# Kernel tuning notes

Hardware: AMD Instinct MI355X
Metric: run time of the kernel (lower is better)

## Reference

```python
import jax, jax.numpy as jnp
import numpy as np

D_MODEL = 1024
N_HEADS = 16
D_HEAD = D_MODEL // N_HEADS
ROPE_BASE = 10000.0


def _rotate_half(x):
    half = x.shape[-1] // 2
    x1, x2 = x[..., :half], x[..., half:]
    return jnp.concatenate([-x2, x1], axis=-1)


def _rope_cos_sin(seq_len, d_head, dtype):
    inv_freq = 1.0 / (ROPE_BASE ** (jnp.arange(0, d_head, 2, dtype=jnp.float32) / d_head))
    t = jnp.arange(seq_len, dtype=jnp.float32)
    freqs = jnp.outer(t, inv_freq)                       # [S, d_head/2]
    emb = jnp.concatenate([freqs, freqs], axis=-1)       # [S, d_head]
    return jnp.cos(emb).astype(dtype), jnp.sin(emb).astype(dtype)


def setup_inputs() -> dict:
    key = jax.random.key(0)
    k1, k2, k3 = jax.random.split(key, 3)
    B, S = 2, 2048
    x = jax.random.normal(k1, (B, S, D_MODEL), dtype=jnp.float32)
    # torch nn.Linear weight layout: [out_features, in_features], y = x @ W.T
    w_qkv = jax.random.normal(k2, (3 * D_MODEL, D_MODEL), dtype=jnp.float32) * (D_MODEL ** -0.5)
    w_out = jax.random.normal(k3, (D_MODEL, D_MODEL), dtype=jnp.float32) * (D_MODEL ** -0.5)
    return {"x": x, "w_qkv": w_qkv, "w_out": w_out}


def reference(x, w_qkv, w_out):
    B, S, _ = x.shape
    qkv = jnp.einsum('bsd,ed->bse', x, w_qkv)            # [B, S, 3*D]
    qkv = qkv.reshape(B, S, 3, N_HEADS, D_HEAD)
    qkv = jnp.transpose(qkv, (2, 0, 3, 1, 4))            # [3, B, H, S, Dh]
    q, k, v = qkv[0], qkv[1], qkv[2]

    cos, sin = _rope_cos_sin(S, D_HEAD, x.dtype)         # [S, Dh] each
    cos = cos[None, None]                                # [1, 1, S, Dh]
    sin = sin[None, None]
    q = q * cos + _rotate_half(q) * sin
    k = k * cos + _rotate_half(k) * sin

    scale = 1.0 / jnp.sqrt(jnp.array(D_HEAD, dtype=x.dtype))
    attn = jnp.einsum('bhqd,bhkd->bhqk', q, k) * scale   # [B, H, S, S]
    causal = jnp.tril(jnp.ones((S, S), dtype=bool))      # triu(diag=1) masked -> keep lower tri
    attn = jnp.where(causal[None, None], attn, jnp.finfo(x.dtype).min)
    attn = jax.nn.softmax(attn, axis=-1)

    out = jnp.einsum('bhqk,bhkd->bhqd', attn, v)         # [B, H, S, Dh]
    out = jnp.transpose(out, (0, 2, 1, 3)).reshape(B, S, D_MODEL)
    return jnp.einsum('bsd,ed->bse', out, w_out)         # out_proj
```

## Files before the change

### kernel.cpp

```cpp
#include <hip/hip_runtime.h>
#include <hip/hip_bf16.h>
#include <cmath>

#define DMODEL 1024
#define NH 16
#define DH 64
#define SEQ 2048
#define BATCH 2

typedef __attribute__((ext_vector_type(8))) short bf16x8;
typedef __attribute__((ext_vector_type(4))) float f32x4;
typedef __attribute__((ext_vector_type(4))) unsigned int u32x4;
typedef __attribute__((ext_vector_type(8))) unsigned short u16x8;

__device__ __forceinline__ unsigned short f2bf(float f) {
    unsigned int u = __builtin_bit_cast(unsigned int, f);
    u += 0x7fffu + ((u >> 16) & 1u);
    return (unsigned short)(u >> 16);
}
__device__ __forceinline__ float exp2_fast(float x) {
    float r;
    asm("v_exp_f32 %0, %1" : "=v"(r) : "v"(x));
    return r;
}

__global__ __launch_bounds__(256)
void cast_all(const float* __restrict__ x, const float* __restrict__ wq,
              const float* __restrict__ wo, unsigned short* __restrict__ xb,
              unsigned short* __restrict__ wqb, unsigned short* __restrict__ wob)
{
    const int i = blockIdx.x * 256 + threadIdx.x;
    const float* src; unsigned short* dst; int off;
    if (i < 524288)      { src = x;  dst = xb;  off = i; }
    else if (i < 917504) { src = wq; dst = wqb; off = i - 524288; }
    else                 { src = wo; dst = wob; off = i - 917504; }
    const float4 a = *(const float4*)(src + (size_t)off * 8);
    const float4 b = *(const float4*)(src + (size_t)off * 8 + 4);
    u16x8 o;
    o[0] = f2bf(a.x); o[1] = f2bf(a.y); o[2] = f2bf(a.z); o[3] = f2bf(a.w);
    o[4] = f2bf(b.x); o[5] = f2bf(b.y); o[6] = f2bf(b.z); o[7] = f2bf(b.w);
    *(u16x8*)(dst + (size_t)off * 8) = o;
}

template<int BM, int EPI>
__global__ __launch_bounds__(256)
void gemm_bf16(const unsigned short* __restrict__ A,
               const unsigned short* __restrict__ B,
               float* __restrict__ oc, unsigned short* __restrict__ oq,
               unsigned short* __restrict__ ok, unsigned short* __restrict__ ovt,
               int M, int N)
{
    constexpr int K = 1024;
    constexpr int BK = 32;
    constexpr int NT = K / BK;
    constexpr int FM = BM / 32;
    __shared__ unsigned short As[2][BM * BK];
    __shared__ unsigned short Bs[2][128 * BK];

    const int t  = threadIdx.x;
    const int l  = t & 63;
    const int w  = t >> 6;
    const int g  = l >> 4;
    const int ln = l & 15;
    const int wr = w >> 1, wc = w & 1;
    const int m0 = blockIdx.y * BM;
    const int n0 = blockIdx.x * 128;

    auto stage = [&](int kt, int bufi) {
        #pragma unroll
        for (int i = 0; i < BM / 64; ++i) {
            const int n = i * 256 + t;
            const int r = n >> 2, slot = n & 3;
            const int kk = kt * BK + ((slot ^ ((r >> 1) & 3)) * 8);
            const unsigned short* ga = A + (size_t)(m0 + r) * K + kk;
            __builtin_amdgcn_global_load_lds(
                (const __attribute__((address_space(1))) unsigned int*)ga,
                (__attribute__((address_space(3))) unsigned int*)&As[bufi][n * 8], 16, 0, 0);
        }
        #pragma unroll
        for (int i = 0; i < 2; ++i) {
            const int n = i * 256 + t;
            const int r = n >> 2, slot = n & 3;
            const int kk = kt * BK + ((slot ^ ((r >> 1) & 3)) * 8);
            const unsigned short* gb = B + (size_t)(n0 + r) * K + kk;
            __builtin_amdgcn_global_load_lds(
                (const __attribute__((address_space(1))) unsigned int*)gb,
                (__attribute__((address_space(3))) unsigned int*)&Bs[bufi][n * 8], 16, 0, 0);
        }
    };

    f32x4 acc[FM][4];
    #pragma unroll
    for (int i = 0; i < FM; ++i)
        #pragma unroll
        for (int j = 0; j < 4; ++j) acc[i][j] = (f32x4){0.f, 0.f, 0.f, 0.f};

    const int swz = (g ^ ((ln >> 1) & 3)) << 4;

    stage(0, 0);
    for (int kt = 0; kt < NT; ++kt) {
        __syncthreads();
        if (kt + 1 < NT) stage(kt + 1, (kt + 1) & 1);
        const char* as = (const char*)As[kt & 1];
        const char* bs = (const char*)Bs[kt & 1];
        bf16x8 af[FM], bfr[4];
        #pragma unroll
        for (int fm = 0; fm < FM; ++fm)
            af[fm] = *(const bf16x8*)(as + (wr * (BM / 2) + fm * 16 + ln) * 64 + swz);
        #pragma unroll
        for (int fn = 0; fn < 4; ++fn)
            bfr[fn] = *(const bf16x8*)(bs + (wc * 64 + fn * 16 + ln) * 64 + swz);
        #pragma unroll
        for (int fm = 0; fm < FM; ++fm)
            #pragma unroll
            for (int fn = 0; fn < 4; ++fn)
                acc[fm][fn] = __builtin_amdgcn_mfma_f32_16x16x32_bf16(
                    af[fm], bfr[fn], acc[fm][fn], 0, 0, 0);
    }

    const int rowbase = m0 + wr * (BM / 2);
    const int colbase = n0 + wc * 64;
    if (EPI == 1) {
        #pragma unroll
        for (int fm = 0; fm < FM; ++fm)
            #pragma unroll
            for (int fn = 0; fn < 4; ++fn)
                #pragma unroll
                for (int rr = 0; rr < 4; ++rr) {
                    const int row = rowbase + fm * 16 + g * 4 + rr;
                    oc[(size_t)row * N + colbase + fn * 16 + ln] = acc[fm][fn][rr];
                }
    } else {
        const int which = colbase >> 10;
        const int h = (colbase >> 6) & (NH - 1);
        if (which < 2) {
            unsigned short* dst = which == 0 ? oq : ok;
            const float scale = which == 0 ? 0.18033688011112042f : 1.f;
            const float cexp = -13.287712379549449f / 32.f;
            const float if0 = exp2f((float)ln * cexp);
            const float if1 = exp2f((float)(16 + ln) * cexp);
            #pragma unroll
            for (int fm = 0; fm < FM; ++fm)
                #pragma unroll
                for (int rr = 0; rr < 4; ++rr) {
                    const int row = rowbase + fm * 16 + g * 4 + rr;
                    const int b = row >> 11, s = row & (SEQ - 1);
                    float s0, c0, s1, c1;
                    __sincosf((float)s * if0, &s0, &c0);
                    __sincosf((float)s * if1, &s1, &c1);
                    const float x0 = acc[fm][0][rr], x1 = acc[fm][1][rr];
                    const float x2 = acc[fm][2][rr], x3 = acc[fm][3][rr];
                    const size_t base = (((size_t)b * NH + h) * SEQ + s) * DH;
                    dst[base + ln]      = f2bf((x0 * c0 - x2 * s0) * scale);
                    dst[base + 16 + ln] = f2bf((x1 * c1 - x3 * s1) * scale);
                    dst[base + 32 + ln] = f2bf((x2 * c0 + x0 * s0) * scale);
                    dst[base + 48 + ln] = f2bf((x3 * c1 + x1 * s1) * scale);
                }
        } else {
            #pragma unroll
            for (int fm = 0; fm < FM; ++fm)
                #pragma unroll
                for (int fn = 0; fn < 4; ++fn) {
                    const int row = rowbase + fm * 16 + g * 4;
                    const int b = row >> 11, s = row & (SEQ - 1);
                    const int d = fn * 16 + ln;
                    ushort4 pk;
                    pk.x = f2bf(acc[fm][fn][0]); pk.y = f2bf(acc[fm][fn][1]);
                    pk.z = f2bf(acc[fm][fn][2]); pk.w = f2bf(acc[fm][fn][3]);
                    *(ushort4*)&ovt[(((size_t)b * NH + h) * DH + d) * SEQ + s] = pk;
                }
        }
    }
}

__global__ __launch_bounds__(256)
void attn_mfma(const unsigned short* __restrict__ q,
               const unsigned short* __restrict__ k,
               const unsigned short* __restrict__ vt,
               unsigned short* __restrict__ ob)
{
    __shared__ unsigned short Ks[2][64 * 64];
    __shared__ unsigned short Vs[2][64 * 64];

    const int t  = threadIdx.x;
    const int l  = t & 63;
    const int w  = t >> 6;
    const int g  = l >> 4;
    const int ln = l & 15;
    const int bid = blockIdx.x;
    const int xcd = bid & 7, jj = bid >> 3;
    const int bh = xcd * 4 + (jj >> 4);
    const int pi = jj & 15;
    const int qtA = pi, qtB = 31 - pi;
    const size_t bqk = (size_t)bh * SEQ * DH;
    const size_t bv  = (size_t)bh * DH * SEQ;

    bf16x8 qfA0, qfA1, qfB0, qfB1;
    {
        const unsigned short* qa = q + bqk + (size_t)(qtA * 64 + w * 16 + ln) * DH + g * 8;
        qfA0 = *(const bf16x8*)qa;  qfA1 = *(const bf16x8*)(qa + 32);
        const unsigned short* qb2 = q + bqk + (size_t)(qtB * 64 + w * 16 + ln) * DH + g * 8;
        qfB0 = *(const bf16x8*)qb2; qfB1 = *(const bf16x8*)(qb2 + 32);
    }

    f32x4 aoA[4], aoB[4];
    #pragma unroll
    for (int i = 0; i < 4; ++i) {
        aoA[i] = (f32x4){0.f, 0.f, 0.f, 0.f};
        aoB[i] = (f32x4){0.f, 0.f, 0.f, 0.f};
    }
    float lA = 0.f, lB = 0.f;

    auto stage = [&](int kt, int bufi) {
        #pragma unroll
        for (int rr = 0; rr < 2; ++rr) {
            const int id  = rr * 256 + t;
            const int row = id >> 3, sl = id & 7;
            const int sg  = (row & 3) | (((row >> 3) & 1) << 2);
            const int slg = (sl ^ sg) * 8;
            const unsigned short* gk = k  + bqk + (size_t)(kt * 64 + row) * DH + slg;
            const unsigned short* gv = vt + bv  + (size_t)row * SEQ + kt * 64 + slg;
            __builtin_amdgcn_global_load_lds(
                (const __attribute__((address_space(1))) unsigned int*)gk,
                (__attribute__((address_space(3))) unsigned int*)&Ks[bufi][id * 8], 16, 0, 0);
            __builtin_amdgcn_global_load_lds(
                (const __attribute__((address_space(1))) unsigned int*)gv,
                (__attribute__((address_space(3))) unsigned int*)&Vs[bufi][id * 8], 16, 0, 0);
        }
    };

    const int rowoffK = ((ln >> 2) * 8 + (ln & 3)) * 128;
    const int sK = (ln & 3) | (((ln >> 2) & 1) << 2);
    const int slotK0 = ((g ^ sK) << 4);
    const int slotK1 = (((g + 4) ^ sK) << 4);
    const int sV = (ln & 3) | (((ln >> 3) & 1) << 2);

    auto softmax_tile = [&](f32x4* s, float& l_, bf16x8* pf) {
        const float M2 = 28.853900817779268f;
        float rs = 0.f;
        unsigned int dw[8];
        #pragma unroll
        for (int nb = 0; nb < 4; ++nb) {
            float e[4];
            #pragma unroll
            for (int r = 0; r < 4; ++r)
                e[r] = exp2_fast(s[nb][r] - M2);
            rs += (e[0] + e[1]) + (e[2] + e[3]);
            dw[nb * 2] = __builtin_amdgcn_perm(
                __builtin_bit_cast(unsigned int, e[1]),
                __builtin_bit_cast(unsigned int, e[0]), 0x07060302u);
            dw[nb * 2 + 1] = __builtin_amdgcn_perm(
                __builtin_bit_cast(unsigned int, e[3]),
                __builtin_bit_cast(unsigned int, e[2]), 0x07060302u);
        }
        l_ += rs;
        pf[0] = __builtin_bit_cast(bf16x8, (u32x4){dw[0], dw[1], dw[2], dw[3]});
        pf[1] = __builtin_bit_cast(bf16x8, (u32x4){dw[4], dw[5], dw[6], dw[7]});
    };

    stage(0, 0);
    for (int kt = 0; kt <= qtB; ++kt) {
        __syncthreads();
        if (kt < qtB) stage(kt + 1, (kt + 1) & 1);
        const bool actA = (kt <= qtA);
        const char* kb = (const char*)Ks[kt & 1];
        const char* vb = (const char*)Vs[kt & 1];

        f32x4 sA[4], sB[4];
        #pragma unroll
        for (int nb = 0; nb < 4; ++nb) {
            sA[nb] = (f32x4){0.f, 0.f, 0.f, 0.f};
            sB[nb] = (f32x4){0.f, 0.f, 0.f, 0.f};
        }
        __builtin_amdgcn_s_setprio(1);
        #pragma unroll
        for (int nb = 0; nb < 4; ++nb) {
            const char* kr = kb + ((nb >> 1) * 32 + (nb & 1) * 4) * 128 + rowoffK;
            bf16x8 kf0 = *(const bf16x8*)(kr + slotK0);
            bf16x8 kf1 = *(const bf16x8*)(kr + slotK1);
            sB[nb] = __builtin_amdgcn_mfma_f32_16x16x32_bf16(kf0, qfB0, sB[nb], 0, 0, 0);
            sB[nb] = __builtin_amdgcn_mfma_f32_16x16x32_bf16(kf1, qfB1, sB[nb], 0, 0, 0);
            if (actA) {
                sA[nb] = __builtin_amdgcn_mfma_f32_16x16x32_bf16(kf0, qfA0, sA[nb], 0, 0, 0);
                sA[nb] = __builtin_amdgcn_mfma_f32_16x16x32_bf16(kf1, qfA1, sA[nb], 0, 0, 0);
            }
        }
        __builtin_amdgcn_s_setprio(0);

        if (kt == qtB) {
            #pragma unroll
            for (int nb = 0; nb < 4; ++nb)
                #pragma unroll
                for (int r = 0; r < 4; ++r)
                    if ((nb >> 1) * 32 + g * 8 + (nb & 1) * 4 + r > w * 16 + ln)
                        sB[nb][r] = -INFINITY;
        }
        if (kt == qtA) {
            #pragma unroll
            for (int nb = 0; nb < 4; ++nb)
                #pragma unroll
                for (int r = 0; r < 4; ++r)
                    if ((nb >> 1) * 32 + g * 8 + (nb & 1) * 4 + r > w * 16 + ln)
                        sA[nb][r] = -INFINITY;
        }

        bf16x8 pfA[2], pfB[2];
        softmax_tile(sB, lB, pfB);
        if (actA) softmax_tile(sA, lA, pfA);

        __builtin_amdgcn_s_setprio(1);
        #pragma unroll
        for (int ks = 0; ks < 2; ++ks) {
            #pragma unroll
            for (int db = 0; db < 4; ++db) {
                const int d = db * 16 + ln;
                bf16x8 vf = *(const bf16x8*)(vb + d * 128 + (((ks * 4 + g) ^ sV) << 4));
                aoB[db] = __builtin_amdgcn_mfma_f32_16x16x32_bf16(pfB[ks], vf, aoB[db], 0, 0, 0);
                if (actA)
                    aoA[db] = __builtin_amdgcn_mfma_f32_16x16x32_bf16(pfA[ks], vf, aoA[db], 0, 0, 0);
            }
        }
        __builtin_amdgcn_s_setprio(0);
    }

    lA += __shfl_xor(lA, 16); lA += __shfl_xor(lA, 32);
    lB += __shfl_xor(lB, 16); lB += __shfl_xor(lB, 32);
    const int b = bh >> 4, h = bh & (NH - 1);
    const float invA = 1.f / lA, invB = 1.f / lB;
    #pragma unroll
    for (int r = 0; r < 4; ++r) {
        const float iA = __shfl(invA, g * 4 + r);
        const float iB = __shfl(invB, g * 4 + r);
        const size_t rowA = (size_t)(b * SEQ + qtA * 64 + w * 16 + g * 4 + r) * DMODEL + h * DH;
        const size_t rowB = (size_t)(b * SEQ + qtB * 64 + w * 16 + g * 4 + r) * DMODEL + h * DH;
        #pragma unroll
        for (int db = 0; db < 4; ++db) {
            ob[rowA + db * 16 + ln] = f2bf(aoA[db][r] * iA);
            ob[rowB + db * 16 + ln] = f2bf(aoB[db][r] * iB);
        }
    }
}

extern "C" void kernel_launch(void* const* d_in, const int* in_sizes, int n_in,
                              void* d_out, int out_size, void* d_ws, size_t ws_size,
                              hipStream_t stream)
{
    const float* x  = (const float*)d_in[0];
    const float* wq = (const float*)d_in[1];
    const float* wo = (const float*)d_in[2];
    float* out = (float*)d_out;

    const size_t NQ = (size_t)BATCH * NH * SEQ * DH;
    unsigned short* qb  = (unsigned short*)d_ws;
    unsigned short* kb  = qb + NQ;
    unsigned short* vtb = kb + NQ;
    unsigned short* ob  = vtb + NQ;
    unsigned short* xb  = ob + NQ;
    unsigned short* wqb = xb + NQ;
    unsigned short* wob = wqb + 3 * DMODEL * DMODEL;

    cast_all<<<4096, 256, 0, stream>>>(x, wq, wo, xb, wqb, wob);

    dim3 g1(3072 / 128, 4096 / 128);
    gemm_bf16<128, 0><<<g1, 256, 0, stream>>>(xb, wqb, nullptr, qb, kb, vtb, 4096, 3072);

    attn_mfma<<<512, 256, 0, stream>>>(qb, kb, vtb, ob);

    dim3 g3(1024 / 128, 4096 / 64);
    gemm_bf16<64, 1><<<g3, 256, 0, stream>>>(ob, wob, out, nullptr, nullptr, nullptr, 4096, 1024);
}
```

Measured before the change: 118.7 us.

## Split paired query tiles across 8 waves instead of per-wave dual tiles

The attention block grows from 256 to 512 threads. Waves 0-3 now handle the short query tile A and waves 4-7 the long tile B, where before each wave computed both tiles. The K/V staging loop is cut to one load per thread and per-wave register pressure drops, which aims at more parallelism and better latency hiding. The cost is that the A waves go idle once their tile ends but still take part in every __syncthreads until tile B is done, so the load is unbalanced within the block.

```diff
diff --git a/kernel.cpp b/kernel.cpp
--- a/kernel.cpp
+++ b/kernel.cpp
@@ -173,7 +173,7 @@
     }
 }
 
-__global__ __launch_bounds__(256)
+__global__ __launch_bounds__(512)
 void attn_mfma(const unsigned short* __restrict__ q,
                const unsigned short* __restrict__ k,
                const unsigned short* __restrict__ vt,
@@ -185,6 +185,7 @@
     const int t  = threadIdx.x;
     const int l  = t & 63;
     const int w  = t >> 6;
+    const int wq = w & 3;
     const int g  = l >> 4;
     const int ln = l & 15;
     const int bid = blockIdx.x;
@@ -192,41 +193,34 @@
     const int bh = xcd * 4 + (jj >> 4);
     const int pi = jj & 15;
     const int qtA = pi, qtB = 31 - pi;
+    const int myqt = (w < 4) ? qtA : qtB;
     const size_t bqk = (size_t)bh * SEQ * DH;
     const size_t bv  = (size_t)bh * DH * SEQ;
 
-    bf16x8 qfA0, qfA1, qfB0, qfB1;
+    bf16x8 qf0, qf1;
     {
-        const unsigned short* qa = q + bqk + (size_t)(qtA * 64 + w * 16 + ln) * DH + g * 8;
-        qfA0 = *(const bf16x8*)qa;  qfA1 = *(const bf16x8*)(qa + 32);
-        const unsigned short* qb2 = q + bqk + (size_t)(qtB * 64 + w * 16 + ln) * DH + g * 8;
-        qfB0 = *(const bf16x8*)qb2; qfB1 = *(const bf16x8*)(qb2 + 32);
-    }
-
-    f32x4 aoA[4], aoB[4];
+        const unsigned short* qp = q + bqk + (size_t)(myqt * 64 + wq * 16 + ln) * DH + g * 8;
+        qf0 = *(const bf16x8*)qp;
+        qf1 = *(const bf16x8*)(qp + 32);
+    }
+
+    f32x4 ao[4];
     #pragma unroll
-    for (int i = 0; i < 4; ++i) {
-        aoA[i] = (f32x4){0.f, 0.f, 0.f, 0.f};
-        aoB[i] = (f32x4){0.f, 0.f, 0.f, 0.f};
-    }
-    float lA = 0.f, lB = 0.f;
+    for (int i = 0; i < 4; ++i) ao[i] = (f32x4){0.f, 0.f, 0.f, 0.f};
+    float l_ = 0.f;
 
     auto stage = [&](int kt, int bufi) {
-        #pragma unroll
-        for (int rr = 0; rr < 2; ++rr) {
-            const int id  = rr * 256 + t;
-            const int row = id >> 3, sl = id & 7;
-            const int sg  = (row & 3) | (((row >> 3) & 1) << 2);
-            const int slg = (sl ^ sg) * 8;
-            const unsigned short* gk = k  + bqk + (size_t)(kt * 64 + row) * DH + slg;
-            const unsigned short* gv = vt + bv  + (size_t)row * SEQ + kt * 64 + slg;
-            __builtin_amdgcn_global_load_lds(
-                (const __attribute__((address_space(1))) unsigned int*)gk,
-                (__attribute__((address_space(3))) unsigned int*)&Ks[bufi][id * 8], 16, 0, 0);
-            __builtin_amdgcn_global_load_lds(
-                (const __attribute__((address_space(1))) unsigned int*)gv,
-                (__attribute__((address_space(3))) unsigned int*)&Vs[bufi][id * 8], 16, 0, 0);
-        }
+        const int row = t >> 3, sl = t & 7;
+        const int sg  = (row & 3) | (((row >> 3) & 1) << 2);
+        const int slg = (sl ^ sg) * 8;
+        const unsigned short* gk = k  + bqk + (size_t)(kt * 64 + row) * DH + slg;
+        const unsigned short* gv = vt + bv  + (size_t)row * SEQ + kt * 64 + slg;
+        __builtin_amdgcn_global_load_lds(
+            (const __attribute__((address_space(1))) unsigned int*)gk,
+            (__attribute__((address_space(3))) unsigned int*)&Ks[bufi][t * 8], 16, 0, 0);
+        __builtin_amdgcn_global_load_lds(
+            (const __attribute__((address_space(1))) unsigned int*)gv,
+            (__attribute__((address_space(3))) unsigned int*)&Vs[bufi][t * 8], 16, 0, 0);
     };
 
     const int rowoffK = ((ln >> 2) * 8 + (ln & 3)) * 128;
@@ -235,109 +229,87 @@
     const int slotK1 = (((g + 4) ^ sK) << 4);
     const int sV = (ln & 3) | (((ln >> 3) & 1) << 2);
 
-    auto softmax_tile = [&](f32x4* s, float& l_, bf16x8* pf) {
-        const float M2 = 28.853900817779268f;
-        float rs = 0.f;
-        unsigned int dw[8];
-        #pragma unroll
-        for (int nb = 0; nb < 4; ++nb) {
-            float e[4];
-            #pragma unroll
-            for (int r = 0; r < 4; ++r)
-                e[r] = exp2_fast(s[nb][r] - M2);
-            rs += (e[0] + e[1]) + (e[2] + e[3]);
-            dw[nb * 2] = __builtin_amdgcn_perm(
-                __builtin_bit_cast(unsigned int, e[1]),
-                __builtin_bit_cast(unsigned int, e[0]), 0x07060302u);
-            dw[nb * 2 + 1] = __builtin_amdgcn_perm(
-                __builtin_bit_cast(unsigned int, e[3]),
-                __builtin_bit_cast(unsigned int, e[2]), 0x07060302u);
-        }
-        l_ += rs;
-        pf[0] = __builtin_bit_cast(bf16x8, (u32x4){dw[0], dw[1], dw[2], dw[3]});
-        pf[1] = __builtin_bit_cast(bf16x8, (u32x4){dw[4], dw[5], dw[6], dw[7]});
-    };
-
     stage(0, 0);
     for (int kt = 0; kt <= qtB; ++kt) {
         __syncthreads();
         if (kt < qtB) stage(kt + 1, (kt + 1) & 1);
-        const bool actA = (kt <= qtA);
+        const bool act = (kt <= myqt);
         const char* kb = (const char*)Ks[kt & 1];
         const char* vb = (const char*)Vs[kt & 1];
 
-        f32x4 sA[4], sB[4];
-        #pragma unroll
-        for (int nb = 0; nb < 4; ++nb) {
-            sA[nb] = (f32x4){0.f, 0.f, 0.f, 0.f};
-            sB[nb] = (f32x4){0.f, 0.f, 0.f, 0.f};
+        if (act) {
+            f32x4 s[4];
+            #pragma unroll
+            for (int nb = 0; nb < 4; ++nb) s[nb] = (f32x4){0.f, 0.f, 0.f, 0.f};
+
+            __builtin_amdgcn_s_setprio(1);
+            #pragma unroll
+            for (int nb = 0; nb < 4; ++nb) {
+                const char* kr = kb + ((nb >> 1) * 32 + (nb & 1) * 4) * 128 + rowoffK;
+                bf16x8 kf0 = *(const bf16x8*)(kr + slotK0);
+                bf16x8 kf1 = *(const bf16x8*)(kr + slotK1);
+                s[nb] = __builtin_amdgcn_mfma_f32_16x16x32_bf16(kf0, qf0, s[nb], 0, 0, 0);
+                s[nb] = __builtin_amdgcn_mfma_f32_16x16x32_bf16(kf1, qf1, s[nb], 0, 0, 0);
+            }
+            __builtin_amdgcn_s_setprio(0);
+
+            if (kt == myqt) {
+                #pragma unroll
+                for (int nb = 0; nb < 4; ++nb)
+                    #pragma unroll
+                    for (int r = 0; r < 4; ++r)
+                        if ((nb >> 1) * 32 + g * 8 + (nb & 1) * 4 + r > wq * 16 + ln)
+                            s[nb][r] = -INFINITY;
+            }
+
+            const float M2 = 28.853900817779268f;
+            bf16x8 pf[2];
+            {
+                float rs = 0.f;
+                unsigned int dw[8];
+                #pragma unroll
+                for (int nb = 0; nb < 4; ++nb) {
+                    float e[4];
+                    #pragma unroll
+                    for (int r = 0; r < 4; ++r)
+                        e[r] = exp2_fast(s[nb][r] - M2);
+                    rs += (e[0] + e[1]) + (e[2] + e[3]);
+                    dw[nb * 2] = __builtin_amdgcn_perm(
+                        __builtin_bit_cast(unsigned int, e[1]),
+                        __builtin_bit_cast(unsigned int, e[0]), 0x07060302u);
+                    dw[nb * 2 + 1] = __builtin_amdgcn_perm(
+                        __builtin_bit_cast(unsigned int, e[3]),
+                        __builtin_bit_cast(unsigned int, e[2]), 0x07060302u);
+                }
+                l_ += rs;
+                pf[0] = __builtin_bit_cast(bf16x8, (u32x4){dw[0], dw[1], dw[2], dw[3]});
+                pf[1] = __builtin_bit_cast(bf16x8, (u32x4){dw[4], dw[5], dw[6], dw[7]});
+            }
+
+            __builtin_amdgcn_s_setprio(1);
+            #pragma unroll
+            for (int ks = 0; ks < 2; ++ks) {
+                #pragma unroll
+                for (int db = 0; db < 4; ++db) {
+                    const int d = db * 16 + ln;
+                    bf16x8 vf = *(const bf16x8*)(vb + d * 128 + (((ks * 4 + g) ^ sV) << 4));
+                    ao[db] = __builtin_amdgcn_mfma_f32_16x16x32_bf16(pf[ks], vf, ao[db], 0, 0, 0);
+                }
+            }
+            __builtin_amdgcn_s_setprio(0);
         }
-        __builtin_amdgcn_s_setprio(1);
-        #pragma unroll
-        for (int nb = 0; nb < 4; ++nb) {
-            const char* kr = kb + ((nb >> 1) * 32 + (nb & 1) * 4) * 128 + rowoffK;
-            bf16x8 kf0 = *(const bf16x8*)(kr + slotK0);
-            bf16x8 kf1 = *(const bf16x8*)(kr + slotK1);
-            sB[nb] = __builtin_amdgcn_mfma_f32_16x16x32_bf16(kf0, qfB0, sB[nb], 0, 0, 0);
-            sB[nb] = __builtin_amdgcn_mfma_f32_16x16x32_bf16(kf1, qfB1, sB[nb], 0, 0, 0);
-            if (actA) {
-                sA[nb] = __builtin_amdgcn_mfma_f32_16x16x32_bf16(kf0, qfA0, sA[nb], 0, 0, 0);
-                sA[nb] = __builtin_amdgcn_mfma_f32_16x16x32_bf16(kf1, qfA1, sA[nb], 0, 0, 0);
-            }
-        }
-        __builtin_amdgcn_s_setprio(0);
-
-        if (kt == qtB) {
-            #pragma unroll
-            for (int nb = 0; nb < 4; ++nb)
-                #pragma unroll
-                for (int r = 0; r < 4; ++r)
-                    if ((nb >> 1) * 32 + g * 8 + (nb & 1) * 4 + r > w * 16 + ln)
-                        sB[nb][r] = -INFINITY;
-        }
-        if (kt == qtA) {
-            #pragma unroll
-            for (int nb = 0; nb < 4; ++nb)
-                #pragma unroll
-                for (int r = 0; r < 4; ++r)
-                    if ((nb >> 1) * 32 + g * 8 + (nb & 1) * 4 + r > w * 16 + ln)
-                        sA[nb][r] = -INFINITY;
-        }
-
-        bf16x8 pfA[2], pfB[2];
-        softmax_tile(sB, lB, pfB);
-        if (actA) softmax_tile(sA, lA, pfA);
-
-        __builtin_amdgcn_s_setprio(1);
-        #pragma unroll
-        for (int ks = 0; ks < 2; ++ks) {
-            #pragma unroll
-            for (int db = 0; db < 4; ++db) {
-                const int d = db * 16 + ln;
-                bf16x8 vf = *(const bf16x8*)(vb + d * 128 + (((ks * 4 + g) ^ sV) << 4));
-                aoB[db] = __builtin_amdgcn_mfma_f32_16x16x32_bf16(pfB[ks], vf, aoB[db], 0, 0, 0);
-                if (actA)
-                    aoA[db] = __builtin_amdgcn_mfma_f32_16x16x32_bf16(pfA[ks], vf, aoA[db], 0, 0, 0);
-            }
-        }
-        __builtin_amdgcn_s_setprio(0);
-    }
-
-    lA += __shfl_xor(lA, 16); lA += __shfl_xor(lA, 32);
-    lB += __shfl_xor(lB, 16); lB += __shfl_xor(lB, 32);
+    }
+
+    l_ += __shfl_xor(l_, 16); l_ += __shfl_xor(l_, 32);
     const int b = bh >> 4, h = bh & (NH - 1);
-    const float invA = 1.f / lA, invB = 1.f / lB;
+    const float inv = 1.f / l_;
     #pragma unroll
     for (int r = 0; r < 4; ++r) {
-        const float iA = __shfl(invA, g * 4 + r);
-        const float iB = __shfl(invB, g * 4 + r);
-        const size_t rowA = (size_t)(b * SEQ + qtA * 64 + w * 16 + g * 4 + r) * DMODEL + h * DH;
-        const size_t rowB = (size_t)(b * SEQ + qtB * 64 + w * 16 + g * 4 + r) * DMODEL + h * DH;
-        #pragma unroll
-        for (int db = 0; db < 4; ++db) {
-            ob[rowA + db * 16 + ln] = f2bf(aoA[db][r] * iA);
-            ob[rowB + db * 16 + ln] = f2bf(aoB[db][r] * iB);
-        }
+        const float iv = __shfl(inv, g * 4 + r);
+        const size_t row = (size_t)(b * SEQ + myqt * 64 + wq * 16 + g * 4 + r) * DMODEL + h * DH;
+        #pragma unroll
+        for (int db = 0; db < 4; ++db)
+            ob[row + db * 16 + ln] = f2bf(ao[db][r] * iv);
     }
 }
 
@@ -364,7 +336,7 @@
     dim3 g1(3072 / 128, 4096 / 128);
     gemm_bf16<128, 0><<<g1, 256, 0, stream>>>(xb, wqb, nullptr, qb, kb, vtb, 4096, 3072);
 
-    attn_mfma<<<512, 256, 0, stream>>>(qb, kb, vtb, ob);
+    attn_mfma<<<512, 512, 0, stream>>>(qb, kb, vtb, ob);
 
     dim3 g3(1024 / 128, 4096 / 64);
     gemm_bf16<64, 1><<<g3, 256, 0, stream>>>(ob, wob, out, nullptr, nullptr, nullptr, 4096, 1024);
```

Measured after the change: 107.5 us. -9.4%, faster.
